# Optimization experiments

Measured on AMD Instinct MI355X. Metric: run time of the kernel, lower is better.

The kernel has to match this reference:

```python
import jax, jax.numpy as jnp
import numpy as np

PS = 4          # patch size
C = 3           # channels
VOCAB = 512
D = 256         # embed dim
PD = PS * PS * C  # 48 patch dim


def _gelu(x):
    return jax.nn.gelu(x, approximate=False)  # torch nn.GELU default = exact erf


def setup_inputs() -> dict:
    key = jax.random.key(0)
    ks = jax.random.split(key, 16)
    frames = jax.random.uniform(ks[0], (32, 256, 256, 3), jnp.float32) * 255.0

    def lin(kw, kb, fan_in, fan_out):
        bound = 1.0 / np.sqrt(fan_in)
        w = jax.random.uniform(kw, (fan_out, fan_in), jnp.float32, -bound, bound)
        b = jax.random.uniform(kb, (fan_out,), jnp.float32, -bound, bound)
        return w, b

    enc_w1, enc_b1 = lin(ks[1], ks[2], PD, D)
    enc_w2, enc_b2 = lin(ks[3], ks[4], D, D)
    enc_w3, enc_b3 = lin(ks[5], ks[6], D, D)
    dec_w1, dec_b1 = lin(ks[7], ks[8], D, D)
    dec_w2, dec_b2 = lin(ks[9], ks[10], D, D)
    dec_w3, dec_b3 = lin(ks[11], ks[12], D, PD)
    codebook = jax.random.normal(ks[13], (VOCAB, D), jnp.float32) * 0.1
    return {
        'frames': frames,
        'enc_w1': enc_w1, 'enc_b1': enc_b1,
        'enc_w2': enc_w2, 'enc_b2': enc_b2,
        'enc_w3': enc_w3, 'enc_b3': enc_b3,
        'codebook': codebook,
        'dec_w1': dec_w1, 'dec_b1': dec_b1,
        'dec_w2': dec_w2, 'dec_b2': dec_b2,
        'dec_w3': dec_w3, 'dec_b3': dec_b3,
    }


def _patchify(x):  # [B,H,W,C] -> [B, N, ps*ps*C]
    B, H, W, Ch = x.shape
    h, w = H // PS, W // PS
    x = x.reshape(B, h, PS, w, PS, Ch).transpose(0, 1, 3, 2, 4, 5)
    return x.reshape(B, h * w, PS * PS * Ch)


def _unpatchify(p):  # [B, N, ps*ps*C] -> [B,H,W,C]
    B, N, _ = p.shape
    h = w = int(np.sqrt(N))
    p = p.reshape(B, h, w, PS, PS, C).transpose(0, 1, 3, 2, 4, 5)
    return p.reshape(B, h * PS, w * PS, C)


def reference(frames, enc_w1, enc_b1, enc_w2, enc_b2, enc_w3, enc_b3,
              codebook, dec_w1, dec_b1, dec_w2, dec_b2, dec_w3, dec_b3):
    x = frames / 255.0 * 2.0 - 1.0
    patches = _patchify(x)  # [B,N,48]
    # encoder MLP
    z = _gelu(patches @ enc_w1.T + enc_b1)
    z = _gelu(z @ enc_w2.T + enc_b2)
    z_e = z @ enc_w3.T + enc_b3  # [B,N,D]
    # nearest-codebook lookup (squared L2; argmin equals cdist argmin)
    d2 = (jnp.sum(z_e * z_e, -1, keepdims=True)
          - 2.0 * jnp.einsum('bnd,vd->bnv', z_e, codebook)
          + jnp.sum(codebook * codebook, -1))  # [B,N,V]
    tokens = jnp.argmin(d2, axis=-1)  # [B,N] int
    z_q = codebook[tokens]  # [B,N,D]
    z_q_st = z_e + jax.lax.stop_gradient(z_q - z_e)
    # decoder MLP
    y = _gelu(z_q_st @ dec_w1.T + dec_b1)
    y = _gelu(y @ dec_w2.T + dec_b2)
    y = y @ dec_w3.T + dec_b3  # [B,N,48]
    recon = _unpatchify(y)
    target = frames / 255.0 * 2.0 - 1.0
    recon_loss = jnp.mean((recon - target) ** 2)
    commitment_loss = jnp.mean((z_e - jax.lax.stop_gradient(z_q)) ** 2)
    codebook_loss = jnp.mean((z_q - jax.lax.stop_gradient(z_e)) ** 2)
    return recon, tokens, recon_loss, commitment_loss, codebook_loss
```

## Files before the change

kernel.cpp:

```cpp
#include <hip/hip_runtime.h>
#include <hip/hip_bf16.h>
#include <math.h>
#include <float.h>
#include <limits.h>

#define T_ROWS 131072

typedef __attribute__((ext_vector_type(8))) short short8;
typedef __attribute__((ext_vector_type(4))) float f32x4;

__device__ __forceinline__ float gelu_f(float x){
    return 0.5f * x * (1.0f + erff(x * 0.7071067811865475f));
}
__device__ __forceinline__ float bf2f(ushort u){
    union { unsigned int i; float f; } v; v.i = ((unsigned int)u) << 16; return v.f;
}
__device__ __forceinline__ ushort f2bf(float f){
    union { float f; unsigned int i; } v; v.f = f;
    unsigned int i = v.i;
    unsigned int r = (i + 0x7fffu + ((i >> 16) & 1u)) >> 16;
    return (ushort)r;
}
__device__ __forceinline__ void split3(float x, ushort &u0, ushort &u1, ushort &u2){
    union { float f; unsigned int i; } v; v.f = x;
    u0 = (ushort)(v.i >> 16);
    union { unsigned int i; float f; } h0; h0.i = ((unsigned int)u0) << 16;
    float r = x - h0.f;
    union { float f; unsigned int i; } vr; vr.f = r;
    u1 = (ushort)(vr.i >> 16);
    union { unsigned int i; float f; } h1; h1.i = ((unsigned int)u1) << 16;
    float r2 = r - h1.f;
    union { float f; unsigned int i; } v2; v2.f = r2;
    u2 = (ushort)(v2.i >> 16);
}

__global__ __launch_bounds__(256) void prep_kernel(
    const float* __restrict__ w2, const float* __restrict__ w3,
    const float* __restrict__ d1, const float* __restrict__ d2,
    const float* __restrict__ w1, const float* __restrict__ b1,
    const float* __restrict__ cb,
    ushort* __restrict__ w2s0, ushort* __restrict__ w2s1, ushort* __restrict__ w2s2,
    ushort* __restrict__ w3s0, ushort* __restrict__ w3s1, ushort* __restrict__ w3s2,
    ushort* __restrict__ w1b, ushort* __restrict__ w2b,
    float* __restrict__ cn, ushort* __restrict__ cbb,
    ushort* __restrict__ cbs0, ushort* __restrict__ cbs1, ushort* __restrict__ cbs2,
    ushort* __restrict__ w1p0, ushort* __restrict__ w1p1, ushort* __restrict__ w1p2,
    float* __restrict__ bias2)
{
    const int blk = blockIdx.x, tid = threadIdx.x;
    if (blk < 64){
        const int i = (blk*256 + tid)*4;
        float4 a = *(const float4*)(w2 + i);
        ushort4 s0, s1, s2;
        split3(a.x, s0.x, s1.x, s2.x); split3(a.y, s0.y, s1.y, s2.y);
        split3(a.z, s0.z, s1.z, s2.z); split3(a.w, s0.w, s1.w, s2.w);
        *(ushort4*)(w2s0+i)=s0; *(ushort4*)(w2s1+i)=s1; *(ushort4*)(w2s2+i)=s2;
        float4 b = *(const float4*)(w3 + i);
        split3(b.x, s0.x, s1.x, s2.x); split3(b.y, s0.y, s1.y, s2.y);
        split3(b.z, s0.z, s1.z, s2.z); split3(b.w, s0.w, s1.w, s2.w);
        *(ushort4*)(w3s0+i)=s0; *(ushort4*)(w3s1+i)=s1; *(ushort4*)(w3s2+i)=s2;
        float4 c = *(const float4*)(d1 + i);
        ushort4 u; u.x=f2bf(c.x); u.y=f2bf(c.y); u.z=f2bf(c.z); u.w=f2bf(c.w);
        *(ushort4*)(w1b+i) = u;
        float4 d = *(const float4*)(d2 + i);
        u.x=f2bf(d.x); u.y=f2bf(d.y); u.z=f2bf(d.z); u.w=f2bf(d.w);
        *(ushort4*)(w2b+i) = u;
    } else if (blk < 192){
        const int lane = tid & 63;
        const int code = (blk-64)*4 + (tid >> 6);
        float4 v = ((const float4*)(cb + (size_t)code*256))[lane];
        size_t off = (size_t)code*256 + lane*4;
        ushort4 u; u.x=f2bf(v.x); u.y=f2bf(v.y); u.z=f2bf(v.z); u.w=f2bf(v.w);
        *(ushort4*)(cbb + off) = u;
        ushort4 s0, s1, s2;
        split3(v.x, s0.x, s1.x, s2.x); split3(v.y, s0.y, s1.y, s2.y);
        split3(v.z, s0.z, s1.z, s2.z); split3(v.w, s0.w, s1.w, s2.w);
        *(ushort4*)(cbs0 + off) = s0;
        *(ushort4*)(cbs1 + off) = s1;
        *(ushort4*)(cbs2 + off) = s2;
        float s = v.x*v.x + v.y*v.y + v.z*v.z + v.w*v.w;
        #pragma unroll
        for (int m=1; m<64; m<<=1) s += __shfl_xor(s, m);
        if (lane == 0) cn[code] = s;
    } else if (blk < 208){
        const int idx = (blk-192)*256 + tid;
        const int n = idx >> 4, k = (idx & 15)*4;
        ushort4 s0 = {0,0,0,0}, s1 = {0,0,0,0}, s2 = {0,0,0,0};
        if (k < 48){
            float4 v = *(const float4*)(w1 + n*48 + k);
            split3(v.x, s0.x, s1.x, s2.x); split3(v.y, s0.y, s1.y, s2.y);
            split3(v.z, s0.z, s1.z, s2.z); split3(v.w, s0.w, s1.w, s2.w);
        }
        *(ushort4*)(w1p0 + n*64 + k) = s0;
        *(ushort4*)(w1p1 + n*64 + k) = s1;
        *(ushort4*)(w1p2 + n*64 + k) = s2;
    } else {
        float s = 0.0f;
        for (int k=0;k<48;++k) s += w1[tid*48 + k];
        bias2[tid] = b1[tid] - s;
    }
}

template<int KTOT, bool GELU, int LOADER, bool SCALE>
__global__ __launch_bounds__(256, 3) void split6_gemm(
    const float* __restrict__ Ain,
    const float* __restrict__ frames,
    const ushort* __restrict__ W0, const ushort* __restrict__ W1,
    const ushort* __restrict__ W2,
    const float* __restrict__ bias,
    float* __restrict__ Cout)
{
    __shared__ __align__(16) ushort Al[3][64][40];
    __shared__ __align__(16) ushort Wl[256][40];

    const int tid = threadIdx.x;
    const int m0 = blockIdx.x * 64;
    const int arow = tid >> 2, q = tid & 3;
    const int lane = tid & 63;
    const int w = tid >> 6;
    const int lr = lane & 15, lg = lane >> 4;

    const float* asrc = nullptr;
    int pbase = 0;
    if constexpr (LOADER == 0){
        asrc = Ain + (size_t)(m0 + arow)*KTOT + q*8;
    } else {
        int p = m0 + arow;
        int b = p >> 12, nl = p & 4095, hh = nl >> 6, ww = nl & 63;
        pbase = ((b*256 + hh*4)*256 + ww*4)*3;
    }
    const ushort* wsrc  = W0 + (size_t)tid*KTOT;
    const ushort* w1frag = W1 + (size_t)(w*64 + lr)*KTOT + lg*8;
    const ushort* w2frag = W2 + (size_t)(w*64 + lr)*KTOT + lg*8;

    f32x4 acc[4][4];
    #pragma unroll
    for (int mi=0;mi<4;++mi)
        #pragma unroll
        for (int ni=0;ni<4;++ni)
            acc[mi][ni] = (f32x4){0.f,0.f,0.f,0.f};

    for (int k0=0; k0<KTOT; k0+=32){
        float x[8];
        if constexpr (LOADER == 0){
            *(float4*)&x[0] = *(const float4*)(asrc + k0);
            *(float4*)&x[4] = *(const float4*)(asrc + k0 + 4);
        } else {
            #pragma unroll
            for (int j=0;j<2;++j){
                int kk = k0 + q*8 + j*4;
                float4 v = {0.f,0.f,0.f,0.f};
                if (kk < 48){
                    int ph = kk/12, rem = kk - ph*12;
                    v = *(const float4*)(frames + pbase + ph*768 + rem);
                }
                x[j*4+0]=v.x; x[j*4+1]=v.y; x[j*4+2]=v.z; x[j*4+3]=v.w;
            }
        }
        ushort t0[8], t1[8], t2[8];
        #pragma unroll
        for (int e=0;e<8;++e) split3(x[e], t0[e], t1[e], t2[e]);
        *(uint4*)&Al[0][arow][q*8] = *(const uint4*)t0;
        *(uint4*)&Al[1][arow][q*8] = *(const uint4*)t1;
        *(uint4*)&Al[2][arow][q*8] = *(const uint4*)t2;
        *(uint4*)&Wl[tid][0]  = *(const uint4*)(wsrc + k0);
        *(uint4*)&Wl[tid][8]  = *(const uint4*)(wsrc + k0 + 8);
        *(uint4*)&Wl[tid][16] = *(const uint4*)(wsrc + k0 + 16);
        *(uint4*)&Wl[tid][24] = *(const uint4*)(wsrc + k0 + 24);
        short8 b1v[4], b2v[4];
        #pragma unroll
        for (int ni=0;ni<4;++ni){
            b1v[ni] = *(const short8*)(w1frag + (size_t)ni*16*KTOT + k0);
            b2v[ni] = *(const short8*)(w2frag + (size_t)ni*16*KTOT + k0);
        }
        __syncthreads();

        short8 b0v[4];
        #pragma unroll
        for (int ni=0;ni<4;++ni)
            b0v[ni] = *(const short8*)&Wl[w*64 + ni*16 + lr][lg*8];
        #pragma unroll
        for (int mi=0;mi<4;++mi){
            short8 a0 = *(const short8*)&Al[0][mi*16 + lr][lg*8];
            short8 a1 = *(const short8*)&Al[1][mi*16 + lr][lg*8];
            short8 a2 = *(const short8*)&Al[2][mi*16 + lr][lg*8];
            #pragma unroll
            for (int ni=0;ni<4;++ni)
                acc[mi][ni] = __builtin_amdgcn_mfma_f32_16x16x32_bf16(a0, b0v[ni], acc[mi][ni], 0,0,0);
            #pragma unroll
            for (int ni=0;ni<4;++ni)
                acc[mi][ni] = __builtin_amdgcn_mfma_f32_16x16x32_bf16(a0, b1v[ni], acc[mi][ni], 0,0,0);
            #pragma unroll
            for (int ni=0;ni<4;++ni)
                acc[mi][ni] = __builtin_amdgcn_mfma_f32_16x16x32_bf16(a1, b0v[ni], acc[mi][ni], 0,0,0);
            #pragma unroll
            for (int ni=0;ni<4;++ni)
                acc[mi][ni] = __builtin_amdgcn_mfma_f32_16x16x32_bf16(a0, b2v[ni], acc[mi][ni], 0,0,0);
            #pragma unroll
            for (int ni=0;ni<4;++ni)
                acc[mi][ni] = __builtin_amdgcn_mfma_f32_16x16x32_bf16(a1, b1v[ni], acc[mi][ni], 0,0,0);
            #pragma unroll
            for (int ni=0;ni<4;++ni)
                acc[mi][ni] = __builtin_amdgcn_mfma_f32_16x16x32_bf16(a2, b0v[ni], acc[mi][ni], 0,0,0);
        }
        __syncthreads();
    }

    const float alpha = 2.0f/255.0f;
    float bn[4];
    #pragma unroll
    for (int ni=0;ni<4;++ni) bn[ni] = bias[w*64 + ni*16 + lr];
    #pragma unroll
    for (int mi=0;mi<4;++mi)
        #pragma unroll
        for (int ni=0;ni<4;++ni)
            #pragma unroll
            for (int r=0;r<4;++r){
                int row = m0 + mi*16 + lg*4 + r;
                float v;
                if (SCALE) v = fmaf(alpha, acc[mi][ni][r], bn[ni]);
                else       v = acc[mi][ni][r] + bn[ni];
                if (GELU) v = gelu_f(v);
                Cout[(size_t)row*256 + w*64 + ni*16 + lr] = v;
            }
}

#define INSERT1(dv, iv) do { \
    float _d = (dv); int _i = (iv); \
    if (_d < bd || (_d == bd && _i < bi)){ bd = _d; bi = _i; } \
} while(0)

__global__ __launch_bounds__(256, 3) void tokens_split6(
    const float* __restrict__ Zf,
    const ushort* __restrict__ C0, const ushort* __restrict__ C1,
    const ushort* __restrict__ C2,
    const float* __restrict__ cn,
    float2* __restrict__ partials,
    float* __restrict__ zz_out)
{
    __shared__ __align__(16) ushort Al[3][64][40];
    __shared__ __align__(16) ushort Wl[256][40];
    __shared__ float2 ptop[64][4];

    const int tid = threadIdx.x;
    const int m0 = blockIdx.x * 64;
    const int cbk = blockIdx.y;
    const int n0 = cbk * 256;
    const int arow = tid >> 2, q = tid & 3;
    const int lane = tid & 63;
    const int w = tid >> 6;
    const int lr = lane & 15, lg = lane >> 4;

    const float*  asrc = Zf + (size_t)(m0 + arow)*256 + q*8;
    const ushort* wsrc = C0 + (size_t)(n0 + tid)*256;
    const ushort* c1frag = C1 + (size_t)(n0 + w*64 + lr)*256 + lg*8;
    const ushort* c2frag = C2 + (size_t)(n0 + w*64 + lr)*256 + lg*8;

    f32x4 acc[4][4];
    #pragma unroll
    for (int mi=0;mi<4;++mi)
        #pragma unroll
        for (int ni=0;ni<4;++ni)
            acc[mi][ni] = (f32x4){0.f,0.f,0.f,0.f};

    float zzp = 0.0f;

    for (int k0=0; k0<256; k0+=32){
        float x[8];
        *(float4*)&x[0] = *(const float4*)(asrc + k0);
        *(float4*)&x[4] = *(const float4*)(asrc + k0 + 4);
        ushort t0[8], t1[8], t2[8];
        #pragma unroll
        for (int e=0;e<8;++e){
            split3(x[e], t0[e], t1[e], t2[e]);
            zzp = fmaf(x[e], x[e], zzp);
        }
        *(uint4*)&Al[0][arow][q*8] = *(const uint4*)t0;
        *(uint4*)&Al[1][arow][q*8] = *(const uint4*)t1;
        *(uint4*)&Al[2][arow][q*8] = *(const uint4*)t2;
        *(uint4*)&Wl[tid][0]  = *(const uint4*)(wsrc + k0);
        *(uint4*)&Wl[tid][8]  = *(const uint4*)(wsrc + k0 + 8);
        *(uint4*)&Wl[tid][16] = *(const uint4*)(wsrc + k0 + 16);
        *(uint4*)&Wl[tid][24] = *(const uint4*)(wsrc + k0 + 24);
        short8 b1v[4], b2v[4];
        #pragma unroll
        for (int ni=0;ni<4;++ni){
            b1v[ni] = *(const short8*)(c1frag + (size_t)ni*16*256 + k0);
            b2v[ni] = *(const short8*)(c2frag + (size_t)ni*16*256 + k0);
        }
        __syncthreads();

        short8 b0v[4];
        #pragma unroll
        for (int ni=0;ni<4;++ni)
            b0v[ni] = *(const short8*)&Wl[w*64 + ni*16 + lr][lg*8];
        #pragma unroll
        for (int mi=0;mi<4;++mi){
            short8 a0 = *(const short8*)&Al[0][mi*16 + lr][lg*8];
            short8 a1 = *(const short8*)&Al[1][mi*16 + lr][lg*8];
            short8 a2 = *(const short8*)&Al[2][mi*16 + lr][lg*8];
            #pragma unroll
            for (int ni=0;ni<4;++ni)
                acc[mi][ni] = __builtin_amdgcn_mfma_f32_16x16x32_bf16(a0, b0v[ni], acc[mi][ni], 0,0,0);
            #pragma unroll
            for (int ni=0;ni<4;++ni)
                acc[mi][ni] = __builtin_amdgcn_mfma_f32_16x16x32_bf16(a0, b1v[ni], acc[mi][ni], 0,0,0);
            #pragma unroll
            for (int ni=0;ni<4;++ni)
                acc[mi][ni] = __builtin_amdgcn_mfma_f32_16x16x32_bf16(a1, b0v[ni], acc[mi][ni], 0,0,0);
            #pragma unroll
            for (int ni=0;ni<4;++ni)
                acc[mi][ni] = __builtin_amdgcn_mfma_f32_16x16x32_bf16(a0, b2v[ni], acc[mi][ni], 0,0,0);
            #pragma unroll
            for (int ni=0;ni<4;++ni)
                acc[mi][ni] = __builtin_amdgcn_mfma_f32_16x16x32_bf16(a1, b1v[ni], acc[mi][ni], 0,0,0);
            #pragma unroll
            for (int ni=0;ni<4;++ni)
                acc[mi][ni] = __builtin_amdgcn_mfma_f32_16x16x32_bf16(a2, b0v[ni], acc[mi][ni], 0,0,0);
        }
        __syncthreads();
    }

    {
        float s = zzp + __shfl_xor(zzp, 1);
        s += __shfl_xor(s, 2);
        if (cbk == 0 && q == 0) zz_out[m0 + arow] = s;
    }

    float cnl[4];
    #pragma unroll
    for (int ni=0;ni<4;++ni) cnl[ni] = cn[n0 + w*64 + ni*16 + lr];

    #pragma unroll
    for (int mi=0;mi<4;++mi)
        #pragma unroll
        for (int r=0;r<4;++r){
            float bd = FLT_MAX; int bi = INT_MAX;
            #pragma unroll
            for (int ni=0;ni<4;++ni){
                float d = cnl[ni] - 2.0f*acc[mi][ni][r];
                int col = n0 + w*64 + ni*16 + lr;
                INSERT1(d, col);
            }
            #pragma unroll
            for (int m=1; m<16; m<<=1){
                float od = __shfl_xor(bd, m);
                int   oi = __shfl_xor(bi, m);
                INSERT1(od, oi);
            }
            if (lr == 0)
                ptop[mi*16 + lg*4 + r][w] = make_float2(bd, (float)bi);
        }
    __syncthreads();
    if (tid < 64){
        float2 h = ptop[tid][0];
        #pragma unroll
        for (int ww=1; ww<4; ++ww){
            float2 o = ptop[tid][ww];
            if (o.x < h.x) h = o;
        }
        partials[(size_t)(m0 + tid)*2 + cbk] = h;
    }
}

__global__ __launch_bounds__(256) void token_reduce(
    const float* __restrict__ zz_out, const float2* __restrict__ partials,
    float* __restrict__ tokf, float* __restrict__ loss)
{
    const int tid = threadIdx.x;
    const int row = blockIdx.x*256 + tid;
    float2 p0 = partials[(size_t)row*2 + 0];
    float2 p1 = partials[(size_t)row*2 + 1];
    float d = p0.x; int g = (int)p0.y;
    if (p1.x < d || (p1.x == d && (int)p1.y < g)){ d = p1.x; g = (int)p1.y; }
    tokf[row] = (float)g;
    float cs = zz_out[row] + d;
    #pragma unroll
    for (int m=1; m<64; m<<=1) cs += __shfl_xor(cs, m);
    __shared__ float wsum[4];
    const int lane = tid & 63, w = tid >> 6;
    if (lane == 0) wsum[w] = cs;
    __syncthreads();
    if (tid == 0) atomicAdd(loss + 1, wsum[0]+wsum[1]+wsum[2]+wsum[3]);
}

template<int LOADER>
__global__ __launch_bounds__(256) void mfma_gemm(
    const ushort* __restrict__ Abf,
    const ushort* __restrict__ cbb,
    const float* __restrict__ tokf,
    const ushort* __restrict__ Wbf,
    const float* __restrict__ bias,
    ushort* __restrict__ Ybf)
{
    __shared__ __align__(16) ushort Al[128][40];
    __shared__ __align__(16) ushort Wl[128][40];

    const int tid = threadIdx.x;
    const int m0 = blockIdx.x * 128;
    const int n0 = blockIdx.y * 128;
    const int srow = tid >> 1, shalf = (tid & 1) * 16;
    const int lane = tid & 63;
    const int w = tid >> 6;
    const int wm = (w >> 1) * 64, wn = (w & 1) * 64;
    const int lr = lane & 15, lg = lane >> 4;

    const ushort* asrc;
    if constexpr (LOADER == 1){
        int g = (int)tokf[m0 + srow];
        asrc = cbb + (size_t)g*256 + shalf;
    } else {
        asrc = Abf + (size_t)(m0 + srow)*256 + shalf;
    }
    const ushort* wsrc = Wbf + (size_t)(n0 + srow)*256 + shalf;

    f32x4 acc[4][4];
    #pragma unroll
    for (int mi=0;mi<4;++mi)
        #pragma unroll
        for (int ni=0;ni<4;++ni)
            acc[mi][ni] = (f32x4){0.f,0.f,0.f,0.f};

    for (int k0=0; k0<256; k0+=32){
        *(uint4*)&Al[srow][shalf]   = *(const uint4*)(asrc + k0);
        *(uint4*)&Al[srow][shalf+8] = *(const uint4*)(asrc + k0 + 8);
        *(uint4*)&Wl[srow][shalf]   = *(const uint4*)(wsrc + k0);
        *(uint4*)&Wl[srow][shalf+8] = *(const uint4*)(wsrc + k0 + 8);
        __syncthreads();

        short8 af[4], bfr[4];
        #pragma unroll
        for (int mi=0;mi<4;++mi)
            af[mi] = *(const short8*)&Al[wm + mi*16 + lr][lg*8];
        #pragma unroll
        for (int ni=0;ni<4;++ni)
            bfr[ni] = *(const short8*)&Wl[wn + ni*16 + lr][lg*8];
        #pragma unroll
        for (int mi=0;mi<4;++mi)
            #pragma unroll
            for (int ni=0;ni<4;++ni)
                acc[mi][ni] = __builtin_amdgcn_mfma_f32_16x16x32_bf16(
                    af[mi], bfr[ni], acc[mi][ni], 0, 0, 0);
        __syncthreads();
    }

    float bn[4];
    #pragma unroll
    for (int ni=0;ni<4;++ni) bn[ni] = bias[n0 + wn + ni*16 + lr];
    #pragma unroll
    for (int mi=0;mi<4;++mi)
        #pragma unroll
        for (int ni=0;ni<4;++ni)
            #pragma unroll
            for (int r=0;r<4;++r){
                int row = m0 + wm + mi*16 + lg*4 + r;
                float v = acc[mi][ni][r] + bn[ni];
                v = gelu_f(v);
                Ybf[(size_t)row*256 + n0 + wn + ni*16 + lr] = f2bf(v);
            }
}

__global__ __launch_bounds__(256) void dec3_mfma(
    const ushort* __restrict__ Ain, const float* __restrict__ W,
    const float* __restrict__ bias, const float* __restrict__ frames,
    float* __restrict__ recon, float* __restrict__ loss)
{
    __shared__ __align__(16) ushort Al[256][40];
    __shared__ __align__(16) ushort Wl[48][40];

    const int tid = threadIdx.x;
    const int m0 = blockIdx.x * 256;
    const int lane = tid & 63;
    const int w = tid >> 6;
    const int lr = lane & 15, lg = lane >> 4;

    const ushort* asrc = Ain + (size_t)(m0 + tid)*256;

    f32x4 acc[4][3];
    #pragma unroll
    for (int mi=0;mi<4;++mi)
        #pragma unroll
        for (int ni=0;ni<3;++ni)
            acc[mi][ni] = (f32x4){0.f,0.f,0.f,0.f};

    for (int k0=0; k0<256; k0+=32){
        *(uint4*)&Al[tid][0]  = *(const uint4*)(asrc + k0);
        *(uint4*)&Al[tid][8]  = *(const uint4*)(asrc + k0 + 8);
        *(uint4*)&Al[tid][16] = *(const uint4*)(asrc + k0 + 16);
        *(uint4*)&Al[tid][24] = *(const uint4*)(asrc + k0 + 24);
        if (tid < 96){
            const int wrow = tid >> 1, wh = (tid & 1)*16;
            const float* wp = W + (size_t)wrow*256 + k0 + wh;
            float4 f0 = *(const float4*)(wp);
            float4 f1 = *(const float4*)(wp+4);
            float4 f2 = *(const float4*)(wp+8);
            float4 f3 = *(const float4*)(wp+12);
            ushort t[16];
            t[0]=f2bf(f0.x); t[1]=f2bf(f0.y); t[2]=f2bf(f0.z); t[3]=f2bf(f0.w);
            t[4]=f2bf(f1.x); t[5]=f2bf(f1.y); t[6]=f2bf(f1.z); t[7]=f2bf(f1.w);
            t[8]=f2bf(f2.x); t[9]=f2bf(f2.y); t[10]=f2bf(f2.z); t[11]=f2bf(f2.w);
            t[12]=f2bf(f3.x); t[13]=f2bf(f3.y); t[14]=f2bf(f3.z); t[15]=f2bf(f3.w);
            *(uint4*)&Wl[wrow][wh]   = *(const uint4*)&t[0];
            *(uint4*)&Wl[wrow][wh+8] = *(const uint4*)&t[8];
        }
        __syncthreads();

        short8 bfr[3];
        #pragma unroll
        for (int ni=0;ni<3;++ni)
            bfr[ni] = *(const short8*)&Wl[ni*16 + lr][lg*8];
        #pragma unroll
        for (int mi=0;mi<4;++mi){
            short8 af = *(const short8*)&Al[w*64 + mi*16 + lr][lg*8];
            #pragma unroll
            for (int ni=0;ni<3;++ni)
                acc[mi][ni] = __builtin_amdgcn_mfma_f32_16x16x32_bf16(
                    af, bfr[ni], acc[mi][ni], 0, 0, 0);
        }
        __syncthreads();
    }

    float bn[3]; int phv[3], remv[3];
    #pragma unroll
    for (int ni=0;ni<3;++ni){
        int col = ni*16 + lr;
        bn[ni] = bias[col];
        phv[ni] = col / 12;
        remv[ni] = col - phv[ni]*12;
    }
    const float sc = 2.0f/255.0f;
    float ls = 0.0f;
    #pragma unroll
    for (int mi=0;mi<4;++mi)
        #pragma unroll
        for (int ni=0;ni<3;++ni)
            #pragma unroll
            for (int r=0;r<4;++r){
                int p = m0 + w*64 + mi*16 + lg*4 + r;
                int b = p >> 12, nl = p & 4095, hh = nl >> 6, ww = nl & 63;
                size_t addr = (size_t)(((b*256 + hh*4 + phv[ni])*256 + ww*4)*3 + remv[ni]);
                float y = acc[mi][ni][r] + bn[ni];
                float t = frames[addr]*sc - 1.0f;
                float d = y - t;
                ls += d*d;
                recon[addr] = y;
            }

    #pragma unroll
    for (int off=32; off>0; off>>=1) ls += __shfl_down(ls, off);
    __shared__ float wsum[4];
    if (lane == 0) wsum[w] = ls;
    __syncthreads();
    if (tid == 0) atomicAdd(loss + 0, wsum[0]+wsum[1]+wsum[2]+wsum[3]);
}

__global__ void finalize_kernel(float* __restrict__ loss){
    if (threadIdx.x == 0 && blockIdx.x == 0){
        loss[0] = loss[0] * (1.0f/6291456.0f);
        float c = loss[1] * (1.0f/33554432.0f);
        loss[1] = c;
        loss[2] = c;
    }
}

extern "C" void kernel_launch(void* const* d_in, const int* in_sizes, int n_in,
                              void* d_out, int out_size, void* d_ws, size_t ws_size,
                              hipStream_t stream)
{
    (void)in_sizes; (void)n_in; (void)out_size; (void)ws_size;
    const float* frames   = (const float*)d_in[0];
    const float* enc_w1   = (const float*)d_in[1];
    const float* enc_b1   = (const float*)d_in[2];
    const float* enc_w2   = (const float*)d_in[3];
    const float* enc_b2   = (const float*)d_in[4];
    const float* enc_w3   = (const float*)d_in[5];
    const float* enc_b3   = (const float*)d_in[6];
    const float* codebook = (const float*)d_in[7];
    const float* dec_w1   = (const float*)d_in[8];
    const float* dec_b1   = (const float*)d_in[9];
    const float* dec_w2   = (const float*)d_in[10];
    const float* dec_b2   = (const float*)d_in[11];
    const float* dec_w3   = (const float*)d_in[12];
    const float* dec_b3   = (const float*)d_in[13];

    float* P = (float*)d_ws;
    float* Q = P + (size_t)33554432;
    float2* partials = (float2*)(Q + 18000000);
    ushort* Y1 = (ushort*)P;
    ushort* Y2 = (ushort*)Q;

    float* recon = (float*)d_out;
    float* tokf  = recon + 6291456;
    float* loss  = tokf + 131072;
    float*  cn   = recon;
    ushort* cbb  = (ushort*)(recon + 512);
    ushort* w1b  = (ushort*)(recon + 66048);
    ushort* w2b  = (ushort*)(recon + 98816);
    ushort* w2s0 = (ushort*)(recon + 131584);
    ushort* w2s1 = (ushort*)(recon + 164352);
    ushort* w2s2 = (ushort*)(recon + 197120);
    ushort* w3s0 = (ushort*)(recon + 229888);
    ushort* w3s1 = (ushort*)(recon + 262656);
    ushort* w3s2 = (ushort*)(recon + 295424);
    ushort* cbs0 = (ushort*)(recon + 328192);
    ushort* cbs1 = (ushort*)(recon + 393728);
    ushort* cbs2 = (ushort*)(recon + 459264);
    float*  zzb  = recon + 524800;
    ushort* w1p0 = (ushort*)(recon + 655872);
    ushort* w1p1 = (ushort*)(recon + 664064);
    ushort* w1p2 = (ushort*)(recon + 672256);
    float*  bias2 = recon + 680448;

    hipMemsetAsync(loss, 0, 3*sizeof(float), stream);

    dim3 blk(256);
    prep_kernel<<<dim3(209), blk, 0, stream>>>(enc_w2, enc_w3, dec_w1, dec_w2,
        enc_w1, enc_b1, codebook,
        w2s0, w2s1, w2s2, w3s0, w3s1, w3s2, w1b, w2b,
        cn, cbb, cbs0, cbs1, cbs2, w1p0, w1p1, w1p2, bias2);
    split6_gemm<64,  true, 1, true ><<<dim3(T_ROWS/64), blk, 0, stream>>>(nullptr, frames, w1p0, w1p1, w1p2, bias2, P);
    split6_gemm<256, true, 0, false><<<dim3(T_ROWS/64), blk, 0, stream>>>(P, nullptr, w2s0, w2s1, w2s2, enc_b2, Q);
    split6_gemm<256, false,0, false><<<dim3(T_ROWS/64), blk, 0, stream>>>(Q, nullptr, w3s0, w3s1, w3s2, enc_b3, P);
    tokens_split6<<<dim3(T_ROWS/64, 2), blk, 0, stream>>>(P, cbs0, cbs1, cbs2, cn, partials, zzb);
    token_reduce<<<dim3(T_ROWS/256), blk, 0, stream>>>(zzb, partials, tokf, loss);
    mfma_gemm<1><<<dim3(T_ROWS/128, 2), blk, 0, stream>>>(nullptr, cbb, tokf, w1b, dec_b1, Y1);
    mfma_gemm<0><<<dim3(T_ROWS/128, 2), blk, 0, stream>>>(Y1, nullptr, nullptr, w2b, dec_b2, Y2);
    dec3_mfma<<<dim3(T_ROWS/256), blk, 0, stream>>>(Y2, dec_w3, dec_b3, frames, recon, loss);
    finalize_kernel<<<dim3(1), dim3(64), 0, stream>>>(loss);
}
```

Measured before the change: 708.6 us.

## Retile codebook distance kernel to 128x128 blocks with four codebook splits

The token-distance kernel moves from 64-row by 256-code tiles to 128-row by 128-code tiles, with a 2x2 arrangement of waves. Both the hi and mid codebook split planes are now staged in LDS, and the lo plane is read directly into registers. Partial argmins are written for four codebook chunks per row, and the reduce kernel merges all four. The aim is more balanced operand reuse and less per-wave global fragment traffic. In exchange, each activation row is converted to split-bf16 four times instead of twice, and LDS use per block rises.

```diff
diff --git a/kernel.cpp b/kernel.cpp
--- a/kernel.cpp
+++ b/kernel.cpp
@@ -238,23 +238,23 @@
     float2* __restrict__ partials,
     float* __restrict__ zz_out)
 {
-    __shared__ __align__(16) ushort Al[3][64][40];
-    __shared__ __align__(16) ushort Wl[256][40];
-    __shared__ float2 ptop[64][4];
+    __shared__ __align__(16) ushort Al[3][128][40];
+    __shared__ __align__(16) ushort Wl[2][128][40];
+    __shared__ float2 ptop[128][2];
 
     const int tid = threadIdx.x;
-    const int m0 = blockIdx.x * 64;
-    const int cbk = blockIdx.y;
-    const int n0 = cbk * 256;
-    const int arow = tid >> 2, q = tid & 3;
+    const int m0 = blockIdx.x * 128;
+    const int n0 = blockIdx.y * 128;
+    const int srow = tid >> 1, shalf = (tid & 1) * 16;
     const int lane = tid & 63;
     const int w = tid >> 6;
+    const int wm = (w >> 1) * 64, wn = (w & 1) * 64;
     const int lr = lane & 15, lg = lane >> 4;
 
-    const float*  asrc = Zf + (size_t)(m0 + arow)*256 + q*8;
-    const ushort* wsrc = C0 + (size_t)(n0 + tid)*256;
-    const ushort* c1frag = C1 + (size_t)(n0 + w*64 + lr)*256 + lg*8;
-    const ushort* c2frag = C2 + (size_t)(n0 + w*64 + lr)*256 + lg*8;
+    const float*  asrc = Zf + (size_t)(m0 + srow)*256 + shalf;
+    const ushort* ws0  = C0 + (size_t)(n0 + srow)*256 + shalf;
+    const ushort* ws1  = C1 + (size_t)(n0 + srow)*256 + shalf;
+    const ushort* c2frag = C2 + (size_t)(n0 + wn + lr)*256 + lg*8;
 
     f32x4 acc[4][4];
     #pragma unroll
@@ -266,70 +266,75 @@
     float zzp = 0.0f;
 
     for (int k0=0; k0<256; k0+=32){
-        float x[8];
-        *(float4*)&x[0] = *(const float4*)(asrc + k0);
-        *(float4*)&x[4] = *(const float4*)(asrc + k0 + 4);
-        ushort t0[8], t1[8], t2[8];
-        #pragma unroll
-        for (int e=0;e<8;++e){
+        float x[16];
+        *(float4*)&x[0]  = *(const float4*)(asrc + k0);
+        *(float4*)&x[4]  = *(const float4*)(asrc + k0 + 4);
+        *(float4*)&x[8]  = *(const float4*)(asrc + k0 + 8);
+        *(float4*)&x[12] = *(const float4*)(asrc + k0 + 12);
+        ushort t0[16], t1[16], t2[16];
+        #pragma unroll
+        for (int e=0;e<16;++e){
             split3(x[e], t0[e], t1[e], t2[e]);
             zzp = fmaf(x[e], x[e], zzp);
         }
-        *(uint4*)&Al[0][arow][q*8] = *(const uint4*)t0;
-        *(uint4*)&Al[1][arow][q*8] = *(const uint4*)t1;
-        *(uint4*)&Al[2][arow][q*8] = *(const uint4*)t2;
-        *(uint4*)&Wl[tid][0]  = *(const uint4*)(wsrc + k0);
-        *(uint4*)&Wl[tid][8]  = *(const uint4*)(wsrc + k0 + 8);
-        *(uint4*)&Wl[tid][16] = *(const uint4*)(wsrc + k0 + 16);
-        *(uint4*)&Wl[tid][24] = *(const uint4*)(wsrc + k0 + 24);
-        short8 b1v[4], b2v[4];
+        *(uint4*)&Al[0][srow][shalf]   = *(const uint4*)&t0[0];
+        *(uint4*)&Al[0][srow][shalf+8] = *(const uint4*)&t0[8];
+        *(uint4*)&Al[1][srow][shalf]   = *(const uint4*)&t1[0];
+        *(uint4*)&Al[1][srow][shalf+8] = *(const uint4*)&t1[8];
+        *(uint4*)&Al[2][srow][shalf]   = *(const uint4*)&t2[0];
+        *(uint4*)&Al[2][srow][shalf+8] = *(const uint4*)&t2[8];
+        *(uint4*)&Wl[0][srow][shalf]   = *(const uint4*)(ws0 + k0);
+        *(uint4*)&Wl[0][srow][shalf+8] = *(const uint4*)(ws0 + k0 + 8);
+        *(uint4*)&Wl[1][srow][shalf]   = *(const uint4*)(ws1 + k0);
+        *(uint4*)&Wl[1][srow][shalf+8] = *(const uint4*)(ws1 + k0 + 8);
+        short8 b2[4];
+        #pragma unroll
+        for (int ni=0;ni<4;++ni)
+            b2[ni] = *(const short8*)(c2frag + (size_t)ni*16*256 + k0);
+        __syncthreads();
+
+        short8 b0[4], b1[4];
         #pragma unroll
         for (int ni=0;ni<4;++ni){
-            b1v[ni] = *(const short8*)(c1frag + (size_t)ni*16*256 + k0);
-            b2v[ni] = *(const short8*)(c2frag + (size_t)ni*16*256 + k0);
-        }
-        __syncthreads();
-
-        short8 b0v[4];
-        #pragma unroll
-        for (int ni=0;ni<4;++ni)
-            b0v[ni] = *(const short8*)&Wl[w*64 + ni*16 + lr][lg*8];
+            b0[ni] = *(const short8*)&Wl[0][wn + ni*16 + lr][lg*8];
+            b1[ni] = *(const short8*)&Wl[1][wn + ni*16 + lr][lg*8];
+        }
         #pragma unroll
         for (int mi=0;mi<4;++mi){
-            short8 a0 = *(const short8*)&Al[0][mi*16 + lr][lg*8];
-            short8 a1 = *(const short8*)&Al[1][mi*16 + lr][lg*8];
-            short8 a2 = *(const short8*)&Al[2][mi*16 + lr][lg*8];
-            #pragma unroll
-            for (int ni=0;ni<4;++ni)
-                acc[mi][ni] = __builtin_amdgcn_mfma_f32_16x16x32_bf16(a0, b0v[ni], acc[mi][ni], 0,0,0);
-            #pragma unroll
-            for (int ni=0;ni<4;++ni)
-                acc[mi][ni] = __builtin_amdgcn_mfma_f32_16x16x32_bf16(a0, b1v[ni], acc[mi][ni], 0,0,0);
-            #pragma unroll
-            for (int ni=0;ni<4;++ni)
-                acc[mi][ni] = __builtin_amdgcn_mfma_f32_16x16x32_bf16(a1, b0v[ni], acc[mi][ni], 0,0,0);
-            #pragma unroll
-            for (int ni=0;ni<4;++ni)
-                acc[mi][ni] = __builtin_amdgcn_mfma_f32_16x16x32_bf16(a0, b2v[ni], acc[mi][ni], 0,0,0);
-            #pragma unroll
-            for (int ni=0;ni<4;++ni)
-                acc[mi][ni] = __builtin_amdgcn_mfma_f32_16x16x32_bf16(a1, b1v[ni], acc[mi][ni], 0,0,0);
-            #pragma unroll
-            for (int ni=0;ni<4;++ni)
-                acc[mi][ni] = __builtin_amdgcn_mfma_f32_16x16x32_bf16(a2, b0v[ni], acc[mi][ni], 0,0,0);
+            short8 a0 = *(const short8*)&Al[0][wm + mi*16 + lr][lg*8];
+            short8 a1 = *(const short8*)&Al[1][wm + mi*16 + lr][lg*8];
+            short8 a2 = *(const short8*)&Al[2][wm + mi*16 + lr][lg*8];
+            #pragma unroll
+            for (int ni=0;ni<4;++ni)
+                acc[mi][ni] = __builtin_amdgcn_mfma_f32_16x16x32_bf16(a0, b0[ni], acc[mi][ni], 0,0,0);
+            #pragma unroll
+            for (int ni=0;ni<4;++ni)
+                acc[mi][ni] = __builtin_amdgcn_mfma_f32_16x16x32_bf16(a0, b1[ni], acc[mi][ni], 0,0,0);
+            #pragma unroll
+            for (int ni=0;ni<4;++ni)
+                acc[mi][ni] = __builtin_amdgcn_mfma_f32_16x16x32_bf16(a1, b0[ni], acc[mi][ni], 0,0,0);
+            #pragma unroll
+            for (int ni=0;ni<4;++ni)
+                acc[mi][ni] = __builtin_amdgcn_mfma_f32_16x16x32_bf16(a0, b2[ni], acc[mi][ni], 0,0,0);
+            #pragma unroll
+            for (int ni=0;ni<4;++ni)
+                acc[mi][ni] = __builtin_amdgcn_mfma_f32_16x16x32_bf16(a1, b1[ni], acc[mi][ni], 0,0,0);
+            #pragma unroll
+            for (int ni=0;ni<4;++ni)
+                acc[mi][ni] = __builtin_amdgcn_mfma_f32_16x16x32_bf16(a2, b0[ni], acc[mi][ni], 0,0,0);
         }
         __syncthreads();
     }
 
     {
-        float s = zzp + __shfl_xor(zzp, 1);
-        s += __shfl_xor(s, 2);
-        if (cbk == 0 && q == 0) zz_out[m0 + arow] = s;
+        float other = __shfl_xor(zzp, 1);
+        if (blockIdx.y == 0 && (tid & 1) == 0)
+            zz_out[m0 + srow] = zzp + other;
     }
 
     float cnl[4];
     #pragma unroll
-    for (int ni=0;ni<4;++ni) cnl[ni] = cn[n0 + w*64 + ni*16 + lr];
+    for (int ni=0;ni<4;++ni) cnl[ni] = cn[n0 + wn + ni*16 + lr];
 
     #pragma unroll
     for (int mi=0;mi<4;++mi)
@@ -339,7 +344,7 @@
             #pragma unroll
             for (int ni=0;ni<4;++ni){
                 float d = cnl[ni] - 2.0f*acc[mi][ni][r];
-                int col = n0 + w*64 + ni*16 + lr;
+                int col = n0 + wn + ni*16 + lr;
                 INSERT1(d, col);
             }
             #pragma unroll
@@ -349,17 +354,14 @@
                 INSERT1(od, oi);
             }
             if (lr == 0)
-                ptop[mi*16 + lg*4 + r][w] = make_float2(bd, (float)bi);
+                ptop[wm + mi*16 + lg*4 + r][w & 1] = make_float2(bd, (float)bi);
         }
     __syncthreads();
-    if (tid < 64){
-        float2 h = ptop[tid][0];
-        #pragma unroll
-        for (int ww=1; ww<4; ++ww){
-            float2 o = ptop[tid][ww];
-            if (o.x < h.x) h = o;
-        }
-        partials[(size_t)(m0 + tid)*2 + cbk] = h;
+    if (tid < 128){
+        float2 hA = ptop[tid][0], hB = ptop[tid][1];
+        int   gA = (int)hA.y, gB = (int)hB.y;
+        bool takeB = (hB.x < hA.x) || (hB.x == hA.x && gB < gA);
+        partials[(size_t)(m0 + tid)*4 + blockIdx.y] = takeB ? hB : hA;
     }
 }
 
@@ -369,10 +371,14 @@
 {
     const int tid = threadIdx.x;
     const int row = blockIdx.x*256 + tid;
-    float2 p0 = partials[(size_t)row*2 + 0];
-    float2 p1 = partials[(size_t)row*2 + 1];
+    float2 p0 = partials[(size_t)row*4 + 0];
+    float2 p1 = partials[(size_t)row*4 + 1];
+    float2 p2 = partials[(size_t)row*4 + 2];
+    float2 p3 = partials[(size_t)row*4 + 3];
     float d = p0.x; int g = (int)p0.y;
     if (p1.x < d || (p1.x == d && (int)p1.y < g)){ d = p1.x; g = (int)p1.y; }
+    if (p2.x < d || (p2.x == d && (int)p2.y < g)){ d = p2.x; g = (int)p2.y; }
+    if (p3.x < d || (p3.x == d && (int)p3.y < g)){ d = p3.x; g = (int)p3.y; }
     tokf[row] = (float)g;
     float cs = zz_out[row] + d;
     #pragma unroll
@@ -621,7 +627,7 @@
     split6_gemm<64,  true, 1, true ><<<dim3(T_ROWS/64), blk, 0, stream>>>(nullptr, frames, w1p0, w1p1, w1p2, bias2, P);
     split6_gemm<256, true, 0, false><<<dim3(T_ROWS/64), blk, 0, stream>>>(P, nullptr, w2s0, w2s1, w2s2, enc_b2, Q);
     split6_gemm<256, false,0, false><<<dim3(T_ROWS/64), blk, 0, stream>>>(Q, nullptr, w3s0, w3s1, w3s2, enc_b3, P);
-    tokens_split6<<<dim3(T_ROWS/64, 2), blk, 0, stream>>>(P, cbs0, cbs1, cbs2, cn, partials, zzb);
+    tokens_split6<<<dim3(T_ROWS/128, 4), blk, 0, stream>>>(P, cbs0, cbs1, cbs2, cn, partials, zzb);
     token_reduce<<<dim3(T_ROWS/256), blk, 0, stream>>>(zzb, partials, tokf, loss);
     mfma_gemm<1><<<dim3(T_ROWS/128, 2), blk, 0, stream>>>(nullptr, cbb, tokf, w1b, dec_b1, Y1);
     mfma_gemm<0><<<dim3(T_ROWS/128, 2), blk, 0, stream>>>(Y1, nullptr, nullptr, w2b, dec_b2, Y2);
```

After: 674.3 us. 1.05x faster.
